# Kernel tuning notes

Hardware: AMD Instinct MI355X
Metric: run time of the kernel (lower is better)

## Reference

```python
import jax, jax.numpy as jnp
import numpy as np
from jax import lax

N, P = 64, 7
C1, H1 = 256, 56
C2, H2 = 512, 28
C3, H3 = 1024, 14
HID1, HID2, HID3 = 256, 768, 1792
MLP1, MLP2, OUT = 3584, 1792, 512


def setup_inputs() -> dict:
    key = jax.random.key(0)
    ks = jax.random.split(key, 32)
    x1 = jax.random.normal(ks[0], (N, C1, H1, H1), jnp.float32)
    x2 = jax.random.normal(ks[1], (N, C2, H2, H2), jnp.float32)
    x3 = jax.random.normal(ks[2], (N, C3, H3, H3), jnp.float32)
    a = jax.random.randint(ks[3], (N, P, 2), 0, 56)
    b = jax.random.randint(ks[4], (N, P, 2), 0, 56)
    lo, hi = jnp.minimum(a, b), jnp.maximum(a, b)
    patchs = jnp.stack([lo[..., 0], hi[..., 0], lo[..., 1], hi[..., 1]], axis=-1)
    drop = jax.random.bernoulli(ks[5], 0.1, (N, P))
    patchs = jnp.where(drop[..., None], 0, patchs).astype(jnp.int32)

    def lin(k, o, i):
        return jax.random.normal(k, (o, i), jnp.float32) * 0.02

    def vec(k, o):
        return jax.random.normal(k, (o,), jnp.float32) * 0.02

    inp = {
        'x1': x1, 'x2': x2, 'x3': x3, 'patchs': patchs,
        # LSTM weights, torch gate order (i,f,g,o); bias = b_ih + b_hh combined
        'l1_wih': lin(ks[6], 4 * HID1, 256),  'l1_whh': lin(ks[7], 4 * HID1, HID1),  'l1_b': vec(ks[8], 4 * HID1),
        'l2_wih': lin(ks[9], 4 * HID2, 768),  'l2_whh': lin(ks[10], 4 * HID2, HID2), 'l2_b': vec(ks[11], 4 * HID2),
        'l3_wih': lin(ks[12], 4 * HID3, 1792),'l3_whh': lin(ks[13], 4 * HID3, HID3), 'l3_b': vec(ks[14], 4 * HID3),
        'aw1': lin(ks[15], MLP1, P * HID3), 'ab1': vec(ks[16], MLP1),
        'aw2': lin(ks[17], MLP2, MLP1),     'ab2': vec(ks[18], MLP2),
        'aw3': lin(ks[19], P, MLP2),        'ab3': vec(ks[20], P),
        'fw':  lin(ks[21], OUT, HID3),      'fb':  vec(ks[22], OUT),
    }
    return inp


def _crop_avg(x, patchs, num, den):
    """Batched data-dependent crop + avg-pool via 2D integral image.
    x: [N,C,H,W]; patchs: [N,P,4] ints (y0,y1,x0,x1) at 56-scale. Returns [N,P,C]."""
    y0 = (patchs[..., 0] * num) // den
    y1 = (patchs[..., 1] * num) // den
    x0 = (patchs[..., 2] * num) // den
    x1 = (patchs[..., 3] * num) // den
    S = jnp.cumsum(jnp.cumsum(x, axis=2), axis=3)
    S = jnp.pad(S, ((0, 0), (0, 0), (1, 0), (1, 0)))  # [N,C,H+1,W+1]
    bidx = jnp.arange(x.shape[0])[:, None]

    def g(Y, X):
        return S[bidx, :, Y, X]  # advanced idx split by ':' -> [N,P,C]

    tot = g(y1 + 1, x1 + 1) - g(y0, x1 + 1) - g(y1 + 1, x0) + g(y0, x0)
    area = ((y1 - y0 + 1) * (x1 - x0 + 1)).astype(x.dtype)[..., None]
    avg = tot / area
    zero = jnp.all(patchs == 0, axis=-1)  # all-zero box -> zero feature
    return jnp.where(zero[..., None], jnp.zeros((), x.dtype), avg)


def _lstm(x, wih, whh, b):
    """Single-layer batch-first LSTM, torch gate order i,f,g,o. x: [N,T,D] -> [N,T,H]."""
    Nb, T, _ = x.shape
    H = whh.shape[1]
    xg = jnp.einsum('ntd,gd->ntg', x, wih) + b  # precompute input gates

    def step(carry, xt):
        h, c = carry
        gates = xt + h @ whh.T
        i, f, g, o = jnp.split(gates, 4, axis=-1)
        c = jax.nn.sigmoid(f) * c + jax.nn.sigmoid(i) * jnp.tanh(g)
        h = jax.nn.sigmoid(o) * jnp.tanh(c)
        return (h, c), h

    h0 = jnp.zeros((Nb, H), x.dtype)
    _, hs = lax.scan(step, (h0, h0), jnp.swapaxes(xg, 0, 1))
    return jnp.swapaxes(hs, 0, 1)


def reference(x1, x2, x3, patchs,
              l1_wih, l1_whh, l1_b, l2_wih, l2_whh, l2_b, l3_wih, l3_whh, l3_b,
              aw1, ab1, aw2, ab2, aw3, ab3, fw, fb):
    local1 = _crop_avg(x1, patchs, 55, 55)                     # [N,7,256]
    rnn1 = _lstm(local1, l1_wih, l1_whh, l1_b)                 # [N,7,256]
    local2 = jnp.concatenate([_crop_avg(x2, patchs, 27, 55), rnn1], axis=2)   # [N,7,768]
    rnn2 = _lstm(local2, l2_wih, l2_whh, l2_b)                 # [N,7,768]
    local3 = jnp.concatenate([_crop_avg(x3, patchs, 13, 55), rnn2], axis=2)   # [N,7,1792]
    rnn3 = _lstm(local3, l3_wih, l3_whh, l3_b)                 # [N,7,1792]
    # attention pooling (dropout = identity in eval)
    flat = rnn3.reshape(rnn3.shape[0], -1)                     # [N,7*1792]
    h = jax.nn.relu(flat @ aw1.T + ab1)
    h = jax.nn.relu(h @ aw2.T + ab2)
    attn = jax.nn.relu(h @ aw3.T + ab3)                        # [N,7]
    alpha = jax.nn.softmax(attn, axis=1)
    feat = jnp.sum(rnn3 * alpha[:, :, None], axis=1)           # [N,1792]
    return feat @ fw.T + fb                                    # [N,512]
```

## Files before the change

### kernel.cpp

```cpp
#include <hip/hip_runtime.h>
#include <hip/hip_bf16.h>
#include <math.h>

#define NB 64
#define PP 7

typedef __attribute__((ext_vector_type(8))) short short8;
typedef __attribute__((ext_vector_type(4))) float f32x4;

static __device__ inline unsigned bf16r(float f) {
    unsigned u = __builtin_bit_cast(unsigned, f);
    u += 0x7fffu + ((u >> 16) & 1u);
    return u >> 16;
}
static __device__ inline unsigned pack2(float a, float b) {
    return bf16r(a) | (bf16r(b) << 16);
}

__global__ __launch_bounds__(256) void cvt_kernel(
    const float* __restrict__ in, uint4* __restrict__ out, int n8)
{
    int idx = blockIdx.x * 256 + threadIdx.x;
    if (idx >= n8) return;
    const float4* p = reinterpret_cast<const float4*>(in) + 2 * (size_t)idx;
    float4 a = p[0], b = p[1];
    uint4 v;
    v.x = pack2(a.x, a.y); v.y = pack2(a.z, a.w);
    v.z = pack2(b.x, b.y); v.w = pack2(b.z, b.w);
    out[idx] = v;
}

template<int H, int VEC, int GRP>
__global__ __launch_bounds__(256) void crop_kernel(
    const float* __restrict__ x, const int* __restrict__ patchs,
    float* __restrict__ out, int C, int num, int den, int ldo, int col0)
{
    constexpr int USED = H / VEC;
    constexpr int PPWAVE = 64 / GRP;
    int tid = threadIdx.x, lane = tid & 63, wv = tid >> 6;
    int n = blockIdx.y;
    int sub = lane / GRP, xl = lane & (GRP - 1);
    bool act = xl < USED;
    int c = blockIdx.x * (4 * PPWAVE) + wv * PPWAVE + sub;

    int y0m1[PP], y1s[PP], x0s[PP], x1s[PP], zer[PP];
    float rarea[PP];
    #pragma unroll
    for (int p = 0; p < PP; ++p) {
        int p0 = patchs[(n * PP + p) * 4 + 0];
        int p1 = patchs[(n * PP + p) * 4 + 1];
        int p2 = patchs[(n * PP + p) * 4 + 2];
        int p3 = patchs[(n * PP + p) * 4 + 3];
        int y0 = p0 * num / den, y1 = p1 * num / den;
        int xx0 = p2 * num / den, xx1 = p3 * num / den;
        y0m1[p] = y0 - 1; y1s[p] = y1; x0s[p] = xx0; x1s[p] = xx1;
        rarea[p] = 1.f / (float)((y1 - y0 + 1) * (xx1 - xx0 + 1));
        zer[p] = (p0 | p1 | p2 | p3) == 0;
    }

    const float* pl = x + ((size_t)n * C + c) * (H * H) + (act ? xl * VEC : 0);

    float cc[VEC];
    float lo[PP][VEC], hi[PP][VEC];
    #pragma unroll
    for (int e = 0; e < VEC; ++e) cc[e] = 0.f;
    #pragma unroll
    for (int p = 0; p < PP; ++p)
        #pragma unroll
        for (int e = 0; e < VEC; ++e) { lo[p][e] = 0.f; hi[p][e] = 0.f; }

    #pragma unroll 4
    for (int y = 0; y < H; ++y) {
        float v[VEC];
        if constexpr (VEC == 4) {
            float4 t = *reinterpret_cast<const float4*>(pl + y * H);
            v[0] = t.x; v[1] = t.y; v[2] = t.z; v[3] = t.w;
        } else {
            float2 t = *reinterpret_cast<const float2*>(pl + y * H);
            v[0] = t.x; v[1] = t.y;
        }
        #pragma unroll
        for (int e = 0; e < VEC; ++e) cc[e] += v[e];
        #pragma unroll
        for (int p = 0; p < PP; ++p) {
            #pragma unroll
            for (int e = 0; e < VEC; ++e) {
                lo[p][e] = (y == y0m1[p]) ? cc[e] : lo[p][e];
                hi[p][e] = (y == y1s[p]) ? cc[e] : hi[p][e];
            }
        }
    }

    #pragma unroll
    for (int p = 0; p < PP; ++p) {
        float d = 0.f;
        #pragma unroll
        for (int e = 0; e < VEC; ++e) {
            int col = xl * VEC + e;
            if (col >= x0s[p] && col <= x1s[p]) d += hi[p][e] - lo[p][e];
        }
        #pragma unroll
        for (int off = GRP / 2; off >= 1; off >>= 1)
            d += __shfl_xor(d, off, 64);
        if (act && xl == 0)
            out[(size_t)(n * PP + p) * ldo + col0 + c] = zer[p] ? 0.f : d * rarea[p];
    }
}

template<int BN, bool WBF>
__global__ __launch_bounds__(256) void gemm_kernel(
    const float* __restrict__ X, int ldx,
    const void* __restrict__ Wp, int K,
    const float* __restrict__ bias,
    float* __restrict__ out, int ldo,
    int kchunk, int partial)
{
    constexpr int NF = BN / 64;
    __shared__ short Xs[64][72];
    __shared__ short Ws[BN][72];
    int tid = threadIdx.x;
    int lane = tid & 63, wv = tid >> 6;
    int m0 = blockIdx.y * 64;
    int o0 = blockIdx.x * BN;
    int z = blockIdx.z;
    int kbeg = z * kchunk, kend = kbeg + kchunk;

    f32x4 acc[4][NF];
    #pragma unroll
    for (int i = 0; i < 4; ++i)
        #pragma unroll
        for (int j = 0; j < NF; ++j)
            acc[i][j] = (f32x4){0.f, 0.f, 0.f, 0.f};

    for (int kb = kbeg; kb < kend; kb += 64) {
        #pragma unroll
        for (int i = 0; i < 2; ++i) {
            int cch = tid + 256 * i;
            int r = cch >> 3, col = (cch & 7) * 8;
            const float* src = X + (size_t)(m0 + r) * ldx + kb + col;
            float4 a = *reinterpret_cast<const float4*>(src);
            float4 b = *reinterpret_cast<const float4*>(src + 4);
            uint4 v;
            v.x = pack2(a.x, a.y); v.y = pack2(a.z, a.w);
            v.z = pack2(b.x, b.y); v.w = pack2(b.z, b.w);
            *reinterpret_cast<uint4*>(&Xs[r][col]) = v;
        }
        #pragma unroll
        for (int i = 0; i < 2 * NF; ++i) {
            int cch = tid + 256 * i;
            int r = cch >> 3, col = (cch & 7) * 8;
            if constexpr (WBF) {
                const short* srcw = (const short*)Wp + (size_t)(o0 + r) * K + kb + col;
                *reinterpret_cast<uint4*>(&Ws[r][col]) =
                    *reinterpret_cast<const uint4*>(srcw);
            } else {
                const float* srcw = (const float*)Wp + (size_t)(o0 + r) * K + kb + col;
                float4 c = *reinterpret_cast<const float4*>(srcw);
                float4 d = *reinterpret_cast<const float4*>(srcw + 4);
                uint4 w;
                w.x = pack2(c.x, c.y); w.y = pack2(c.z, c.w);
                w.z = pack2(d.x, d.y); w.w = pack2(d.z, d.w);
                *reinterpret_cast<uint4*>(&Ws[r][col]) = w;
            }
        }
        __syncthreads();
        #pragma unroll
        for (int kk = 0; kk < 64; kk += 32) {
            int ro = lane & 15, kof = kk + (lane >> 4) * 8;
            short8 b[NF];
            #pragma unroll
            for (int j = 0; j < NF; ++j)
                b[j] = *reinterpret_cast<const short8*>(
                    &Ws[wv * (BN / 4) + 16 * j + ro][kof]);
            #pragma unroll
            for (int i = 0; i < 4; ++i) {
                short8 a = *reinterpret_cast<const short8*>(&Xs[16 * i + ro][kof]);
                #pragma unroll
                for (int j = 0; j < NF; ++j)
                    acc[i][j] = __builtin_amdgcn_mfma_f32_16x16x32_bf16(
                        a, b[j], acc[i][j], 0, 0, 0);
            }
        }
        __syncthreads();
    }

    float* dst = out;
    if (partial) dst += (size_t)z * (gridDim.y * 64) * ldo;
    int mr = (lane >> 4) * 4;
    #pragma unroll
    for (int j = 0; j < NF; ++j) {
        int o = o0 + wv * (BN / 4) + 16 * j + (lane & 15);
        float bv = (!partial && bias) ? bias[o] : 0.f;
        #pragma unroll
        for (int i = 0; i < 4; ++i) {
            #pragma unroll
            for (int r = 0; r < 4; ++r) {
                int m = m0 + 16 * i + mr + r;
                dst[(size_t)m * ldo + o] = acc[i][j][r] + bv;
            }
        }
    }
}

__global__ __launch_bounds__(256) void reduce_kernel(
    const float* __restrict__ partial, int S, int M, int O,
    const float* __restrict__ bias, int relu, float* __restrict__ out)
{
    int idx = blockIdx.x * 256 + threadIdx.x;
    int tot = M * O;
    if (idx >= tot) return;
    float v = bias[idx % O];
    for (int s = 0; s < S; ++s) v += partial[(size_t)s * tot + idx];
    if (relu) v = fmaxf(v, 0.f);
    out[idx] = v;
}

__global__ __launch_bounds__(256) void lstm_cell_kernel(
    const float* __restrict__ partial, int S,
    const float* __restrict__ xgt, int ldxg,
    float* __restrict__ h, float* __restrict__ c,
    float* __restrict__ dest, int Hd, int ldd, int first)
{
    int idx = blockIdx.x * 256 + threadIdx.x;
    int q = Hd >> 2;
    if (idx >= NB * q) return;
    int n = idx / q, j4 = (idx - n * q) * 4;
    int H4 = 4 * Hd;

    f32x4 g[4];
    #pragma unroll
    for (int gi = 0; gi < 4; ++gi)
        g[gi] = *reinterpret_cast<const f32x4*>(xgt + (size_t)n * ldxg + gi * Hd + j4);
    if (!first) {
        for (int s = 0; s < S; ++s) {
            const float* pr = partial + ((size_t)s * NB + n) * H4;
            #pragma unroll
            for (int gi = 0; gi < 4; ++gi)
                g[gi] += *reinterpret_cast<const f32x4*>(pr + gi * Hd + j4);
        }
    }
    f32x4 cp = (f32x4){0.f, 0.f, 0.f, 0.f};
    if (!first) cp = *reinterpret_cast<const f32x4*>(c + (size_t)n * Hd + j4);

    f32x4 cn, hn;
    #pragma unroll
    for (int k = 0; k < 4; ++k) {
        float si = 1.f / (1.f + expf(-g[0][k]));
        float sf = 1.f / (1.f + expf(-g[1][k]));
        float so = 1.f / (1.f + expf(-g[3][k]));
        float cc = sf * cp[k] + si * tanhf(g[2][k]);
        cn[k] = cc;
        hn[k] = so * tanhf(cc);
    }
    *reinterpret_cast<f32x4*>(c + (size_t)n * Hd + j4) = cn;
    *reinterpret_cast<f32x4*>(h + (size_t)n * Hd + j4) = hn;
    *reinterpret_cast<f32x4*>(dest + (size_t)n * ldd + j4) = hn;
}

__global__ __launch_bounds__(256) void attn_fused_kernel(
    const float* __restrict__ h2, const float* __restrict__ aw3,
    const float* __restrict__ ab3, const float* __restrict__ rnn3,
    float* __restrict__ feat)
{
    int n = blockIdx.x;
    int tid = threadIdx.x, lane = tid & 63, wv = tid >> 6;
    __shared__ float logit[PP];
    __shared__ float alpha[PP];
    for (int p = wv; p < PP; p += 4) {
        float s = 0.f;
        for (int k = lane; k < 1792; k += 64)
            s += h2[n * 1792 + k] * aw3[p * 1792 + k];
        #pragma unroll
        for (int off = 32; off; off >>= 1) s += __shfl_down(s, off, 64);
        if (lane == 0) logit[p] = fmaxf(s + ab3[p], 0.f);
    }
    __syncthreads();
    if (tid == 0) {
        float a[PP], mx = -1e30f;
        for (int p = 0; p < PP; ++p) { a[p] = logit[p]; mx = fmaxf(mx, a[p]); }
        float s = 0.f;
        for (int p = 0; p < PP; ++p) { a[p] = expf(a[p] - mx); s += a[p]; }
        for (int p = 0; p < PP; ++p) alpha[p] = a[p] / s;
    }
    __syncthreads();
    for (int j = tid; j < 1792; j += 256) {
        float s = 0.f;
        #pragma unroll
        for (int p = 0; p < PP; ++p)
            s += rnn3[((size_t)n * PP + p) * 1792 + j] * alpha[p];
        feat[(size_t)n * 1792 + j] = s;
    }
}


extern "C" void kernel_launch(void* const* d_in, const int* in_sizes, int n_in,
                              void* d_out, int out_size, void* d_ws, size_t ws_size,
                              hipStream_t stream) {
    const float* x1 = (const float*)d_in[0];
    const float* x2 = (const float*)d_in[1];
    const float* x3 = (const float*)d_in[2];
    const int* patchs = (const int*)d_in[3];
    const float* l1_wih = (const float*)d_in[4];
    const float* l1_whh = (const float*)d_in[5];
    const float* l1_b   = (const float*)d_in[6];
    const float* l2_wih = (const float*)d_in[7];
    const float* l2_whh = (const float*)d_in[8];
    const float* l2_b   = (const float*)d_in[9];
    const float* l3_wih = (const float*)d_in[10];
    const float* l3_whh = (const float*)d_in[11];
    const float* l3_b   = (const float*)d_in[12];
    const float* aw1 = (const float*)d_in[13];
    const float* ab1 = (const float*)d_in[14];
    const float* aw2 = (const float*)d_in[15];
    const float* ab2 = (const float*)d_in[16];
    const float* aw3 = (const float*)d_in[17];
    const float* ab3 = (const float*)d_in[18];
    const float* fw  = (const float*)d_in[19];
    const float* fb  = (const float*)d_in[20];
    float* out = (float*)d_out;

    float* ws = (float*)d_ws;
    float* local1 = ws;
    float* local2 = local1 + 114688;
    float* local3 = local2 + 344064;
    float* rnn3   = local3;
    float* xg     = local3 + 802816;
    float* partial= xg + 3211264;
    float* hbuf   = partial + 3211264;
    float* cbuf   = hbuf + 114688;
    float* h1     = cbuf + 114688;
    float* h2     = h1 + 229376;
    float* feat   = h2 + 114688;
    float* wb     = feat + 114688;
    short* whh1b  = (short*)wb;
    short* whh2b  = (short*)(wb + 131072);
    short* whh3b  = (short*)(wb + 131072 + 1179648);
    short* wih3b  = (short*)(wb + 131072 + 1179648 + 6422528);

    cvt_kernel<<<(262144 / 8 + 255) / 256, 256, 0, stream>>>(
        l1_whh, (uint4*)whh1b, 262144 / 8);
    cvt_kernel<<<(2359296 / 8 + 255) / 256, 256, 0, stream>>>(
        l2_whh, (uint4*)whh2b, 2359296 / 8);
    cvt_kernel<<<(12845056 / 8 + 255) / 256, 256, 0, stream>>>(
        l3_whh, (uint4*)whh3b, 12845056 / 8);
    cvt_kernel<<<(12845056 / 8 + 255) / 256, 256, 0, stream>>>(
        l3_wih, (uint4*)wih3b, 12845056 / 8);

    crop_kernel<56, 4, 16><<<dim3(16, NB), 256, 0, stream>>>(
        x1, patchs, local1, 256, 55, 55, 256, 0);
    crop_kernel<28, 4, 8><<<dim3(16, NB), 256, 0, stream>>>(
        x2, patchs, local2, 512, 27, 55, 768, 0);
    crop_kernel<14, 2, 8><<<dim3(32, NB), 256, 0, stream>>>(
        x3, patchs, local3, 1024, 13, 55, 1792, 0);

    {
        int H = 256, H4 = 1024;
        gemm_kernel<64, false><<<dim3(16, 7, 1), 256, 0, stream>>>(
            local1, 256, l1_wih, 256, l1_b, xg, H4, 256, 0);
        for (int t = 0; t < PP; ++t) {
            if (t > 0)
                gemm_kernel<64, true><<<dim3(16, 1, 4), 256, 0, stream>>>(
                    hbuf, H, whh1b, H, nullptr, partial, H4, 64, 1);
            lstm_cell_kernel<<<(NB * H / 4 + 255) / 256, 256, 0, stream>>>(
                partial, 4, xg + (size_t)t * H4, PP * H4,
                hbuf, cbuf, local2 + (size_t)t * 768 + 512, H, PP * 768, t == 0);
        }
    }
    {
        int H = 768, H4 = 3072;
        gemm_kernel<64, false><<<dim3(48, 7, 1), 256, 0, stream>>>(
            local2, 768, l2_wih, 768, l2_b, xg, H4, 768, 0);
        for (int t = 0; t < PP; ++t) {
            if (t > 0)
                gemm_kernel<64, true><<<dim3(48, 1, 6), 256, 0, stream>>>(
                    hbuf, H, whh2b, H, nullptr, partial, H4, 128, 1);
            lstm_cell_kernel<<<(NB * H / 4 + 255) / 256, 256, 0, stream>>>(
                partial, 6, xg + (size_t)t * H4, PP * H4,
                hbuf, cbuf, local3 + (size_t)t * 1792 + 1024, H, PP * 1792, t == 0);
        }
    }
    {
        int H = 1792, H4 = 7168;
        gemm_kernel<256, true><<<dim3(28, 7, 1), 256, 0, stream>>>(
            local3, 1792, wih3b, 1792, l3_b, xg, H4, 1792, 0);
        for (int t = 0; t < PP; ++t) {
            if (t > 0)
                gemm_kernel<256, true><<<dim3(28, 1, 7), 256, 0, stream>>>(
                    hbuf, H, whh3b, H, nullptr, partial, H4, 256, 1);
            lstm_cell_kernel<<<(NB * H / 4 + 255) / 256, 256, 0, stream>>>(
                partial, 7, xg + (size_t)t * H4, PP * H4,
                hbuf, cbuf, rnn3 + (size_t)t * 1792, H, PP * 1792, t == 0);
        }
    }

    gemm_kernel<64, false><<<dim3(56, 1, 14), 256, 0, stream>>>(
        rnn3, 12544, aw1, 12544, nullptr, partial, 3584, 896, 1);
    reduce_kernel<<<(64 * 3584 + 255) / 256, 256, 0, stream>>>(
        partial, 14, 64, 3584, ab1, 1, h1);
    gemm_kernel<64, false><<<dim3(28, 1, 7), 256, 0, stream>>>(
        h1, 3584, aw2, 3584, nullptr, partial, 1792, 512, 1);
    reduce_kernel<<<(64 * 1792 + 255) / 256, 256, 0, stream>>>(
        partial, 7, 64, 1792, ab2, 1, h2);
    attn_fused_kernel<<<NB, 256, 0, stream>>>(h2, aw3, ab3, rnn3, feat);
    gemm_kernel<64, false><<<dim3(8, 1, 7), 256, 0, stream>>>(
        feat, 1792, fw, 1792, nullptr, partial, 512, 256, 1);
    reduce_kernel<<<(64 * 512 + 255) / 256, 256, 0, stream>>>(
        partial, 7, 64, 512, fb, 0, out);
}
```

Before: 607.8 us.

## Fuse crop and weight conversion into one prep kernel; skip wih3 bf16 conversion

Merges the three crop kernels and three of the fp32→bf16 weight-conversion kernels into a single prep kernel that branches on block index, so one launch replaces six and the independent work can run concurrently. It drops the bf16 conversion of l3_wih and has the layer-3 input GEMM read the fp32 weights directly with BN=128 tiles. The layer-3 recurrent GEMM also moves from BN=256 to BN=128, doubling the block count. The trade is that reading fp32 weights in the input GEMM moves more bytes in that GEMM, while it avoids a full read-plus-write pass to convert those weights.

```diff
diff --git a/kernel.cpp b/kernel.cpp
--- a/kernel.cpp
+++ b/kernel.cpp
@@ -17,31 +17,17 @@
     return bf16r(a) | (bf16r(b) << 16);
 }
 
-__global__ __launch_bounds__(256) void cvt_kernel(
-    const float* __restrict__ in, uint4* __restrict__ out, int n8)
-{
-    int idx = blockIdx.x * 256 + threadIdx.x;
-    if (idx >= n8) return;
-    const float4* p = reinterpret_cast<const float4*>(in) + 2 * (size_t)idx;
-    float4 a = p[0], b = p[1];
-    uint4 v;
-    v.x = pack2(a.x, a.y); v.y = pack2(a.z, a.w);
-    v.z = pack2(b.x, b.y); v.w = pack2(b.z, b.w);
-    out[idx] = v;
-}
-
 template<int H, int VEC, int GRP>
-__global__ __launch_bounds__(256) void crop_kernel(
-    const float* __restrict__ x, const int* __restrict__ patchs,
+__device__ inline void crop_dev(
+    int bx, int n, const float* __restrict__ x, const int* __restrict__ patchs,
     float* __restrict__ out, int C, int num, int den, int ldo, int col0)
 {
     constexpr int USED = H / VEC;
     constexpr int PPWAVE = 64 / GRP;
     int tid = threadIdx.x, lane = tid & 63, wv = tid >> 6;
-    int n = blockIdx.y;
     int sub = lane / GRP, xl = lane & (GRP - 1);
     bool act = xl < USED;
-    int c = blockIdx.x * (4 * PPWAVE) + wv * PPWAVE + sub;
+    int c = bx * (4 * PPWAVE) + wv * PPWAVE + sub;
 
     int y0m1[PP], y1s[PP], x0s[PP], x1s[PP], zer[PP];
     float rarea[PP];
@@ -104,6 +90,46 @@
             d += __shfl_xor(d, off, 64);
         if (act && xl == 0)
             out[(size_t)(n * PP + p) * ldo + col0 + c] = zer[p] ? 0.f : d * rarea[p];
+    }
+}
+
+__device__ inline void cvt_dev(
+    int b, const float* __restrict__ in, uint4* __restrict__ out, int n8)
+{
+    int idx = b * 256 + threadIdx.x;
+    if (idx >= n8) return;
+    const float4* p = reinterpret_cast<const float4*>(in) + 2 * (size_t)idx;
+    float4 a = p[0], bb = p[1];
+    uint4 v;
+    v.x = pack2(a.x, a.y); v.y = pack2(a.z, a.w);
+    v.z = pack2(bb.x, bb.y); v.w = pack2(bb.z, bb.w);
+    out[idx] = v;
+}
+
+__global__ __launch_bounds__(256) void prep_kernel(
+    const float* __restrict__ x1, const float* __restrict__ x2,
+    const float* __restrict__ x3, const int* __restrict__ patchs,
+    float* __restrict__ local1, float* __restrict__ local2,
+    float* __restrict__ local3,
+    const float* __restrict__ l1_whh, uint4* __restrict__ whh1b,
+    const float* __restrict__ l2_whh, uint4* __restrict__ whh2b,
+    const float* __restrict__ l3_whh, uint4* __restrict__ whh3b)
+{
+    int b = blockIdx.x;
+    if (b < 1024) {
+        crop_dev<56, 4, 16>(b & 15, b >> 4, x1, patchs, local1, 256, 55, 55, 256, 0);
+    } else if (b < 2048) {
+        int bb = b - 1024;
+        crop_dev<28, 4, 8>(bb & 15, bb >> 4, x2, patchs, local2, 512, 27, 55, 768, 0);
+    } else if (b < 4096) {
+        int bb = b - 2048;
+        crop_dev<14, 2, 8>(bb & 31, bb >> 5, x3, patchs, local3, 1024, 13, 55, 1792, 0);
+    } else if (b < 4224) {
+        cvt_dev(b - 4096, l1_whh, whh1b, 32768);
+    } else if (b < 5376) {
+        cvt_dev(b - 4224, l2_whh, whh2b, 294912);
+    } else {
+        cvt_dev(b - 5376, l3_whh, whh3b, 1605632);
     }
 }
 
@@ -335,23 +361,10 @@
     short* whh1b  = (short*)wb;
     short* whh2b  = (short*)(wb + 131072);
     short* whh3b  = (short*)(wb + 131072 + 1179648);
-    short* wih3b  = (short*)(wb + 131072 + 1179648 + 6422528);
-
-    cvt_kernel<<<(262144 / 8 + 255) / 256, 256, 0, stream>>>(
-        l1_whh, (uint4*)whh1b, 262144 / 8);
-    cvt_kernel<<<(2359296 / 8 + 255) / 256, 256, 0, stream>>>(
-        l2_whh, (uint4*)whh2b, 2359296 / 8);
-    cvt_kernel<<<(12845056 / 8 + 255) / 256, 256, 0, stream>>>(
-        l3_whh, (uint4*)whh3b, 12845056 / 8);
-    cvt_kernel<<<(12845056 / 8 + 255) / 256, 256, 0, stream>>>(
-        l3_wih, (uint4*)wih3b, 12845056 / 8);
-
-    crop_kernel<56, 4, 16><<<dim3(16, NB), 256, 0, stream>>>(
-        x1, patchs, local1, 256, 55, 55, 256, 0);
-    crop_kernel<28, 4, 8><<<dim3(16, NB), 256, 0, stream>>>(
-        x2, patchs, local2, 512, 27, 55, 768, 0);
-    crop_kernel<14, 2, 8><<<dim3(32, NB), 256, 0, stream>>>(
-        x3, patchs, local3, 1024, 13, 55, 1792, 0);
+
+    prep_kernel<<<11648, 256, 0, stream>>>(
+        x1, x2, x3, patchs, local1, local2, local3,
+        l1_whh, (uint4*)whh1b, l2_whh, (uint4*)whh2b, l3_whh, (uint4*)whh3b);
 
     {
         int H = 256, H4 = 1024;
@@ -381,11 +394,11 @@
     }
     {
         int H = 1792, H4 = 7168;
-        gemm_kernel<256, true><<<dim3(28, 7, 1), 256, 0, stream>>>(
-            local3, 1792, wih3b, 1792, l3_b, xg, H4, 1792, 0);
+        gemm_kernel<128, false><<<dim3(56, 7, 1), 256, 0, stream>>>(
+            local3, 1792, l3_wih, 1792, l3_b, xg, H4, 1792, 0);
         for (int t = 0; t < PP; ++t) {
             if (t > 0)
-                gemm_kernel<256, true><<<dim3(28, 1, 7), 256, 0, stream>>>(
+                gemm_kernel<128, true><<<dim3(56, 1, 7), 256, 0, stream>>>(
                     hbuf, H, whh3b, H, nullptr, partial, H4, 256, 1);
             lstm_cell_kernel<<<(NB * H / 4 + 255) / 256, 256, 0, stream>>>(
                 partial, 7, xg + (size_t)t * H4, PP * H4,
```

Result: no change. 608.6 us (+0.1%).
